# Optimization experiments

Hardware: AMD Instinct MI355X
Metric: run time of the kernel (lower is better)

## Reference

```python
import jax, jax.numpy as jnp
import numpy as np

DIM = 768
DEPTH = 12
HEADS = 12
DIM_HEAD = DIM // HEADS
DIM_MLP = 3072
PATCH = 16
SPECTRA = 4096
NUM_PATCHES = SPECTRA // PATCH
NUM_CLASSES = 1000
SCALE = DIM_HEAD ** -0.5
EPS = 1e-5


def sincos_pos_embed(embed_dim, n_pos):
    omega = np.arange(embed_dim // 2, dtype=np.float64) / (embed_dim / 2.0)
    omega = 1.0 / 10000 ** omega
    pos = np.arange(n_pos, dtype=np.float64)
    out = np.einsum('m,d->md', pos, omega)
    emb = np.concatenate([np.sin(out), np.cos(out)], axis=1)
    emb = np.concatenate([np.zeros([1, embed_dim]), emb], axis=0)  # cls slot
    return jnp.asarray(emb, jnp.float32)  # [N+1, D]


def setup_inputs() -> dict:
    key = jax.random.key(0)
    ks = jax.random.split(key, 12)
    s = 0.02
    d = {
        'x': jax.random.normal(ks[0], (32, 1, SPECTRA), jnp.float32),
        'conv_w': jax.random.normal(ks[1], (PATCH, DIM), jnp.float32) * s,
        'conv_b': jnp.zeros((DIM,), jnp.float32),
        'pos_embed': sincos_pos_embed(DIM, NUM_PATCHES),
        'cls_token': jax.random.normal(ks[2], (1, DIM), jnp.float32) * s,
        'ln1_w': jnp.ones((DEPTH, DIM), jnp.float32),
        'ln1_b': jnp.zeros((DEPTH, DIM), jnp.float32),
        'qkv_w': jax.random.normal(ks[3], (DEPTH, DIM, 3 * DIM), jnp.float32) * s,
        'out_w': jax.random.normal(ks[4], (DEPTH, DIM, DIM), jnp.float32) * s,
        'out_b': jnp.zeros((DEPTH, DIM), jnp.float32),
        'ln2_w': jnp.ones((DEPTH, DIM), jnp.float32),
        'ln2_b': jnp.zeros((DEPTH, DIM), jnp.float32),
        'mlp_w1': jax.random.normal(ks[5], (DEPTH, DIM, DIM_MLP), jnp.float32) * s,
        'mlp_b1': jnp.zeros((DEPTH, DIM_MLP), jnp.float32),
        'mlp_w2': jax.random.normal(ks[6], (DEPTH, DIM_MLP, DIM), jnp.float32) * s,
        'mlp_b2': jnp.zeros((DEPTH, DIM), jnp.float32),
        'cls_ln_w': jnp.ones((DIM,), jnp.float32),
        'cls_ln_b': jnp.zeros((DIM,), jnp.float32),
        'head_w': jax.random.normal(ks[7], (DIM, NUM_CLASSES), jnp.float32) * s,
        'head_b': jnp.zeros((NUM_CLASSES,), jnp.float32),
    }
    return d


def _ln(z, w, b):
    mu = z.mean(-1, keepdims=True)
    var = ((z - mu) ** 2).mean(-1, keepdims=True)
    return (z - mu) / jnp.sqrt(var + EPS) * w + b


def _forward(x, conv_w, conv_b, pos_embed, cls_token,
             ln1_w, ln1_b, qkv_w, out_w, out_b, ln2_w, ln2_b,
             mlp_w1, mlp_b1, mlp_w2, mlp_b2,
             cls_ln_w, cls_ln_b, head_w, head_b):
    B = x.shape[0]
    # Conv1d(1, D, k=P, stride=P) == non-overlapping patch linear proj
    patches = x.reshape(B, NUM_PATCHES, PATCH)
    h = patches @ conv_w + conv_b                         # [B, N, D]
    h = h + pos_embed[1:]
    cls = cls_token + pos_embed[:1]                       # [1, D]
    h = jnp.concatenate([jnp.broadcast_to(cls[None], (B, 1, DIM)), h], axis=1)  # [B, N+1, D]

    def block(h, p):
        l1w, l1b, qw, ow, ob, l2w, l2b, w1, b1, w2, b2 = p
        skip = h
        z = _ln(h, l1w, l1b)
        qkv = z @ qw                                      # [B, n, 3D]
        q, k, v = jnp.split(qkv, 3, axis=-1)
        def heads(t):
            return t.reshape(B, -1, HEADS, DIM_HEAD).transpose(0, 2, 1, 3)
        q, k, v = heads(q), heads(k), heads(v)            # [B, H, n, dh]
        dots = jnp.einsum('bhid,bhjd->bhij', q, k) * SCALE
        attn = jax.nn.softmax(dots, axis=-1)
        o = jnp.einsum('bhij,bhjd->bhid', attn, v)
        o = o.transpose(0, 2, 1, 3).reshape(B, -1, DIM)
        h = o @ ow + ob + skip
        skip = h
        z = _ln(h, l2w, l2b)
        z = jax.nn.gelu(z @ w1 + b1, approximate=False) @ w2 + b2
        return z + skip, None

    params = (ln1_w, ln1_b, qkv_w, out_w, out_b, ln2_w, ln2_b,
              mlp_w1, mlp_b1, mlp_w2, mlp_b2)
    h, _ = jax.lax.scan(block, h, params)
    cls_out = _ln(h[:, 0], cls_ln_w, cls_ln_b)
    return cls_out @ head_w + head_b                      # [B, num_classes]


def reference(x, conv_w, conv_b, pos_embed, cls_token,
              ln1_w, ln1_b, qkv_w, out_w, out_b, ln2_w, ln2_b,
              mlp_w1, mlp_b1, mlp_w2, mlp_b2,
              cls_ln_w, cls_ln_b, head_w, head_b):
    return _forward(x, conv_w, conv_b, pos_embed, cls_token,
                    ln1_w, ln1_b, qkv_w, out_w, out_b, ln2_w, ln2_b,
                    mlp_w1, mlp_b1, mlp_w2, mlp_b2,
                    cls_ln_w, cls_ln_b, head_w, head_b)
```

## Files before the change

kernel.cpp:

```cpp
#include <hip/hip_runtime.h>
#include <math.h>

#define DIM 768
#define DEPTH 12
#define HEADS 12
#define DIM_HEAD 64
#define DIM_MLP 3072
#define PATCH 16
#define NUM_PATCHES 256
#define SEQ 257
#define NUM_CLASSES 1000
#define BATCH 32
#define SCALE 0.125f
#define EPS 1e-5f
#define ROWS 8224
#define PAD_ROWS 8320
#define PAD_A 8448

typedef short bf16x8 __attribute__((ext_vector_type(8)));
typedef float f32x4 __attribute__((ext_vector_type(4)));

__device__ inline unsigned short f2bf(float f) {
    union { float f; unsigned int u; } c; c.f = f;
    unsigned int u = c.u;
    return (unsigned short)((u + 0x7fffu + ((u >> 16) & 1u)) >> 16);
}

#define MFMA16(d, a, b) d = __builtin_amdgcn_mfma_f32_16x16x32_bf16(a, b, d, 0, 0, 0)
#define SBAR() asm volatile("s_barrier" ::: "memory")
#define LGKM0() asm volatile("s_waitcnt lgkmcnt(0)" ::: "memory")

__global__ void patch_embed_kernel(const float* __restrict__ x,
                                   const float* __restrict__ conv_w,
                                   const float* __restrict__ conv_b,
                                   const float* __restrict__ pos,
                                   const float* __restrict__ cls_tok,
                                   float* __restrict__ h) {
    int row = blockIdx.x;
    int b = row / SEQ;
    int r = row % SEQ;
    int t = threadIdx.x;
    float* out = h + (long)row * DIM;
    if (r == 0) {
        for (int d = t; d < DIM; d += 256)
            out[d] = cls_tok[d] + pos[d];
        return;
    }
    int p = r - 1;
    const float* xp = x + (long)b * 4096 + p * PATCH;
    float xv[PATCH];
#pragma unroll
    for (int k = 0; k < PATCH; ++k) xv[k] = xp[k];
    for (int d = t; d < DIM; d += 256) {
        float acc = conv_b[d];
#pragma unroll
        for (int k = 0; k < PATCH; ++k)
            acc += xv[k] * conv_w[k * DIM + d];
        out[d] = acc + pos[(long)r * DIM + d];
    }
}

template <int OBF>
__global__ void layernorm_kernel(const float* __restrict__ in, long in_stride,
                                 const float* __restrict__ w,
                                 const float* __restrict__ bia,
                                 void* __restrict__ out) {
    __shared__ float red[8];
    long row = blockIdx.x;
    const float* src = in + row * in_stride;
    int t = threadIdx.x;
    float v0 = src[t], v1 = src[t + 256], v2 = src[t + 512];
    float s = v0 + v1 + v2;
    float q = v0 * v0 + v1 * v1 + v2 * v2;
#pragma unroll
    for (int off = 32; off; off >>= 1) {
        s += __shfl_down(s, off);
        q += __shfl_down(q, off);
    }
    if ((t & 63) == 0) { red[t >> 6] = s; red[4 + (t >> 6)] = q; }
    __syncthreads();
    if (t == 0) {
        float ss = red[0] + red[1] + red[2] + red[3];
        float qq = red[4] + red[5] + red[6] + red[7];
        float mu = ss * (1.0f / DIM);
        float var = qq * (1.0f / DIM) - mu * mu;
        red[0] = mu;
        red[1] = rsqrtf(var + EPS);
    }
    __syncthreads();
    float mu = red[0], rstd = red[1];
    float o0 = (v0 - mu) * rstd * w[t] + bia[t];
    float o1 = (v1 - mu) * rstd * w[t + 256] + bia[t + 256];
    float o2 = (v2 - mu) * rstd * w[t + 512] + bia[t + 512];
    if (OBF) {
        unsigned short* dst = (unsigned short*)out + row * DIM;
        dst[t] = f2bf(o0); dst[t + 256] = f2bf(o1); dst[t + 512] = f2bf(o2);
    } else {
        float* dst = (float*)out + row * DIM;
        dst[t] = o0; dst[t + 256] = o1; dst[t + 512] = o2;
    }
}

__global__ void transpose_all_kernel(const float* __restrict__ qw,
                                     const float* __restrict__ ow,
                                     const float* __restrict__ w1,
                                     const float* __restrict__ w2,
                                     unsigned short* __restrict__ qwT,
                                     unsigned short* __restrict__ owT,
                                     unsigned short* __restrict__ w1T,
                                     unsigned short* __restrict__ w2T) {
    __shared__ float tile[32][33];
    int t = blockIdx.x;
    const float* src; unsigned short* dst; int K, N, kt, nt;
    if (t < 1728)      {            src = qw; dst = qwT; K = 768;  N = 2304; kt = t % 24; nt = t / 24; }
    else if (t < 2304) { t -= 1728; src = ow; dst = owT; K = 768;  N = 768;  kt = t % 24; nt = t / 24; }
    else if (t < 4608) { t -= 2304; src = w1; dst = w1T; K = 768;  N = 3072; kt = t % 24; nt = t / 24; }
    else               { t -= 4608; src = w2; dst = w2T; K = 3072; N = 768;  kt = t % 96; nt = t / 96; }
    int k0 = kt * 32, n0 = nt * 32;
    int c = threadIdx.x & 31, r0 = threadIdx.x >> 5;
#pragma unroll
    for (int rr = r0; rr < 32; rr += 8)
        tile[rr][c] = src[(long)(k0 + rr) * N + n0 + c];
    __syncthreads();
#pragma unroll
    for (int rr = r0; rr < 32; rr += 8)
        dst[(long)(n0 + rr) * K + k0 + c] = f2bf(tile[c][rr]);
}

__global__ __launch_bounds__(256) void attn_kernel(const unsigned short* __restrict__ qkv,
                                                   unsigned short* __restrict__ o) {
    __shared__ unsigned short sh[60416];
    const int tid = threadIdx.x;
    const int lane = tid & 63;
    const int w = tid >> 6;

    const int nwg = gridDim.x;
    const int orig = blockIdx.x;
    const int q = nwg >> 3, r = nwg & 7;
    const int xcd = orig & 7, idx = orig >> 3;
    const int wg = (xcd < r ? xcd * (q + 1) : r * (q + 1) + (xcd - r) * q) + idx;
    const int bh = wg / 5, qt = wg % 5;
    const int b = bh / HEADS, hh = bh % HEADS;
    const unsigned short* qbase = qkv + (long)b * SEQ * 2304 + hh * 64;
    const unsigned short* kbase = qbase + 768;
    const unsigned short* vbase = qbase + 1536;

#pragma unroll
    for (int u = 0; u < 2; ++u) {
        int c = tid + u * 256;
        int j = c >> 3, cb = c & 7;
        int gj = qt * 64 + j; if (gj > 256) gj = 256;
        const unsigned short* g = qbase + (long)gj * 2304 + ((cb ^ (j & 7)) << 3);
        __builtin_amdgcn_global_load_lds(
            (const __attribute__((address_space(1))) void*)g,
            (__attribute__((address_space(3))) void*)&sh[j * 64 + cb * 8], 16, 0, 0);
    }
#pragma unroll
    for (int u = 0; u < 9; ++u) {
        int c = tid + u * 256;
        int j = c >> 3, cb = c & 7;
        int gj = j > 256 ? 256 : j;
        const unsigned short* g = kbase + (long)gj * 2304 + ((cb ^ (j & 7)) << 3);
        __builtin_amdgcn_global_load_lds(
            (const __attribute__((address_space(1))) void*)g,
            (__attribute__((address_space(3))) void*)&sh[4096 + j * 64 + cb * 8], 16, 0, 0);
    }
#pragma unroll
    for (int u = 0; u < 9; ++u) {
        int c = tid + u * 256;
        int j = c >> 3, dc = c & 7;
        short vv[8] = {0, 0, 0, 0, 0, 0, 0, 0};
        if (j < SEQ) *(bf16x8*)vv = *(const bf16x8*)(vbase + (long)j * 2304 + dc * 8);
#pragma unroll
        for (int e = 0; e < 8; ++e)
            sh[22528 + (dc * 8 + e) * 296 + j] = (unsigned short)vv[e];
    }
    __syncthreads();

    f32x4 s[18] = {};
#pragma unroll
    for (int ks = 0; ks < 2; ++ks) {
        int arow = w * 16 + (lane & 15);
        int cb = ks * 4 + (lane >> 4);
        bf16x8 aq = *(const bf16x8*)&sh[arow * 64 + ((cb ^ (arow & 7)) << 3)];
#pragma unroll
        for (int nf = 0; nf < 18; ++nf) {
            int brow = nf * 16 + (lane & 15);
            bf16x8 bk = *(const bf16x8*)&sh[4096 + brow * 64 + ((cb ^ (brow & 7)) << 3)];
            MFMA16(s[nf], aq, bk);
        }
    }

    float inv[4];
#pragma unroll
    for (int j = 0; j < 4; ++j) {
        float m_ = -3.0e38f;
#pragma unroll
        for (int nf = 0; nf < 18; ++nf) {
            int col = nf * 16 + (lane & 15);
            float x = (col < SEQ) ? s[nf][j] * SCALE : -3.0e38f;
            s[nf][j] = x;
            m_ = fmaxf(m_, x);
        }
#pragma unroll
        for (int off = 1; off < 16; off <<= 1) m_ = fmaxf(m_, __shfl_xor(m_, off));
        float sm = 0.f;
#pragma unroll
        for (int nf = 0; nf < 18; ++nf) {
            float e = __expf(s[nf][j] - m_);
            s[nf][j] = e;
            sm += e;
        }
#pragma unroll
        for (int off = 1; off < 16; off <<= 1) sm += __shfl_xor(sm, off);
        inv[j] = 1.0f / sm;
    }
#pragma unroll
    for (int nf = 0; nf < 18; ++nf) {
        int col = nf * 16 + (lane & 15);
#pragma unroll
        for (int j = 0; j < 4; ++j) {
            int row = w * 16 + (lane >> 4) * 4 + j;
            sh[41472 + row * 296 + col] = f2bf(s[nf][j] * inv[j]);
        }
    }
    __syncthreads();

    f32x4 oa[4] = {};
#pragma unroll
    for (int ks = 0; ks < 9; ++ks) {
        int prow = w * 16 + (lane & 15);
        bf16x8 ap = *(const bf16x8*)&sh[41472 + prow * 296 + ks * 32 + (lane >> 4) * 8];
#pragma unroll
        for (int n = 0; n < 4; ++n) {
            int drow = n * 16 + (lane & 15);
            bf16x8 bv = *(const bf16x8*)&sh[22528 + drow * 296 + ks * 32 + (lane >> 4) * 8];
            MFMA16(oa[n], ap, bv);
        }
    }
#pragma unroll
    for (int n = 0; n < 4; ++n) {
        int col = hh * 64 + n * 16 + (lane & 15);
#pragma unroll
        for (int j = 0; j < 4; ++j) {
            int gr = qt * 64 + w * 16 + (lane >> 4) * 4 + j;
            if (gr < SEQ)
                o[((long)(b * SEQ + gr)) * DIM + col] = f2bf(oa[n][j]);
        }
    }
}

template <int NK, int ACT, int OBF>
__global__ __launch_bounds__(256, 2) void gemmd_kernel(
    const unsigned short* __restrict__ A,
    const unsigned short* __restrict__ Bt,
    const float* __restrict__ bias,
    const float* __restrict__ resid,
    void* __restrict__ C,
    int M, int GY, int lda, int ldb, int ldc) {
    __shared__ unsigned short sh[32768];
    const int tid = threadIdx.x;
    const int lane = tid & 63;
    const int w = tid >> 6;
    const int wr = w >> 1, wc = w & 1;

    const int nwg = gridDim.x;
    const int orig = blockIdx.x;
    const int q = nwg >> 3, r = nwg & 7;
    const int xcd = orig & 7, idx = orig >> 3;
    const int wg = (xcd < r ? xcd * (q + 1) : r * (q + 1) + (xcd - r) * q) + idx;
    const int bm = (wg / GY) * 128;
    const int bn = (wg % GY) * 128;

    const unsigned short* Ag = A + (long)bm * lda;
    const unsigned short* Bg = Bt + (long)bn * ldb;

    auto stage = [&](int kt) {
        unsigned short* La = &sh[(kt & 1) * 16384];
        unsigned short* Lb = La + 8192;
#pragma unroll
        for (int u = 0; u < 4; ++u) {
            int c = tid + u * 256;
            int lr = c >> 3, cb = c & 7;
            int sw = (cb ^ (lr & 7)) << 3;
            const unsigned short* ga = Ag + (long)lr * lda + kt * 64 + sw;
            __builtin_amdgcn_global_load_lds(
                (const __attribute__((address_space(1))) void*)ga,
                (__attribute__((address_space(3))) void*)&La[lr * 64 + (cb << 3)], 16, 0, 0);
            const unsigned short* gb = Bg + (long)lr * ldb + kt * 64 + sw;
            __builtin_amdgcn_global_load_lds(
                (const __attribute__((address_space(1))) void*)gb,
                (__attribute__((address_space(3))) void*)&Lb[lr * 64 + (cb << 3)], 16, 0, 0);
        }
    };
    auto ldA = [&](int p, int m, int ks) {
        int row = wr * 64 + m * 16 + (lane & 15);
        int cb = ks * 4 + (lane >> 4);
        return *(const bf16x8*)&sh[p * 16384 + row * 64 + ((cb ^ (row & 7)) << 3)];
    };
    auto ldB = [&](int p, int n, int ks) {
        int row = wc * 64 + n * 16 + (lane & 15);
        int cb = ks * 4 + (lane >> 4);
        return *(const bf16x8*)&sh[p * 16384 + 8192 + row * 64 + ((cb ^ (row & 7)) << 3)];
    };

    f32x4 acc[4][4] = {};

    stage(0); stage(1);
    asm volatile("s_waitcnt vmcnt(8)" ::: "memory");
    SBAR();

    for (int kt = 0; kt < NK; ++kt) {
        const int p = kt & 1;
        bf16x8 a[4][2], b[4][2];
#pragma unroll
        for (int m = 0; m < 4; ++m) { a[m][0] = ldA(p, m, 0); a[m][1] = ldA(p, m, 1); }
#pragma unroll
        for (int n = 0; n < 4; ++n) { b[n][0] = ldB(p, n, 0); b[n][1] = ldB(p, n, 1); }
        SBAR();
        if (kt + 2 < NK) stage(kt + 2);
        LGKM0();
        __builtin_amdgcn_s_setprio(1);
#pragma unroll
        for (int m = 0; m < 4; ++m)
#pragma unroll
            for (int n = 0; n < 4; ++n) {
                MFMA16(acc[m][n], a[m][0], b[n][0]);
                MFMA16(acc[m][n], a[m][1], b[n][1]);
            }
        __builtin_amdgcn_s_setprio(0);
        if (kt + 2 < NK) {
            asm volatile("s_waitcnt vmcnt(8)" ::: "memory");
        } else if (kt + 1 < NK) {
            asm volatile("s_waitcnt vmcnt(0)" ::: "memory");
        }
        SBAR();
    }

#pragma unroll
    for (int mi = 0; mi < 4; ++mi) {
        int gr0 = bm + wr * 64 + mi * 16 + (lane >> 4) * 4;
#pragma unroll
        for (int ni = 0; ni < 4; ++ni) {
            int gc = bn + wc * 64 + ni * 16 + (lane & 15);
            float bv = bias ? bias[gc] : 0.f;
#pragma unroll
            for (int j = 0; j < 4; ++j) {
                int gr = gr0 + j;
                if (gr >= M) continue;
                float v = acc[mi][ni][j] + bv;
                if (ACT) v = 0.5f * v * (1.0f + erff(v * 0.70710678118654752f));
                long ci = (long)gr * ldc + gc;
                if (OBF) {
                    ((unsigned short*)C)[ci] = f2bf(v);
                } else {
                    if (resid) v += resid[ci];
                    ((float*)C)[ci] = v;
                }
            }
        }
    }
}

__global__ void gemm_f32_kernel(const float* __restrict__ A,
                                const float* __restrict__ W,
                                const float* __restrict__ bias,
                                float* __restrict__ C,
                                int M, int N, int K) {
    __shared__ float As[16][65];
    __shared__ float Bs[16][65];
    int bm = blockIdx.x * 64, bn = blockIdx.y * 64;
    int t = threadIdx.x;
    int tx = t & 15, ty = t >> 4;
    float acc[4][4] = {};
    for (int k0 = 0; k0 < K; k0 += 16) {
        {
            int ar = bm + (t >> 2);
            int ac = k0 + (t & 3) * 4;
            float4 av = make_float4(0.f, 0.f, 0.f, 0.f);
            if (ar < M) av = *(const float4*)(A + (long)ar * K + ac);
            int kk = (t & 3) * 4, rr = t >> 2;
            As[kk + 0][rr] = av.x; As[kk + 1][rr] = av.y;
            As[kk + 2][rr] = av.z; As[kk + 3][rr] = av.w;
        }
        {
            int wr2 = k0 + (t >> 4);
            int wc2 = bn + (t & 15) * 4;
            float4 wv;
            wv.x = (wc2 + 0 < N) ? W[(long)wr2 * N + wc2 + 0] : 0.f;
            wv.y = (wc2 + 1 < N) ? W[(long)wr2 * N + wc2 + 1] : 0.f;
            wv.z = (wc2 + 2 < N) ? W[(long)wr2 * N + wc2 + 2] : 0.f;
            wv.w = (wc2 + 3 < N) ? W[(long)wr2 * N + wc2 + 3] : 0.f;
            int kr = t >> 4, nc = (t & 15) * 4;
            Bs[kr][nc + 0] = wv.x; Bs[kr][nc + 1] = wv.y;
            Bs[kr][nc + 2] = wv.z; Bs[kr][nc + 3] = wv.w;
        }
        __syncthreads();
#pragma unroll
        for (int kk = 0; kk < 16; ++kk) {
            float a0 = As[kk][ty * 4 + 0], a1 = As[kk][ty * 4 + 1];
            float a2 = As[kk][ty * 4 + 2], a3 = As[kk][ty * 4 + 3];
            float b0 = Bs[kk][tx], b1 = Bs[kk][tx + 16];
            float b2 = Bs[kk][tx + 32], b3 = Bs[kk][tx + 48];
            acc[0][0] += a0 * b0; acc[0][1] += a0 * b1; acc[0][2] += a0 * b2; acc[0][3] += a0 * b3;
            acc[1][0] += a1 * b0; acc[1][1] += a1 * b1; acc[1][2] += a1 * b2; acc[1][3] += a1 * b3;
            acc[2][0] += a2 * b0; acc[2][1] += a2 * b1; acc[2][2] += a2 * b2; acc[2][3] += a2 * b3;
            acc[3][0] += a3 * b0; acc[3][1] += a3 * b1; acc[3][2] += a3 * b2; acc[3][3] += a3 * b3;
        }
        __syncthreads();
    }
#pragma unroll
    for (int i = 0; i < 4; ++i) {
        int r = bm + ty * 4 + i;
        if (r >= M) continue;
#pragma unroll
        for (int j = 0; j < 4; ++j) {
            int c = bn + tx + 16 * j;
            if (c >= N) continue;
            C[(long)r * N + c] = acc[i][j] + (bias ? bias[c] : 0.f);
        }
    }
}

extern "C" void kernel_launch(void* const* d_in, const int* in_sizes, int n_in,
                              void* d_out, int out_size, void* d_ws, size_t ws_size,
                              hipStream_t stream) {
    const float* x        = (const float*)d_in[0];
    const float* conv_w   = (const float*)d_in[1];
    const float* conv_b   = (const float*)d_in[2];
    const float* pos      = (const float*)d_in[3];
    const float* cls_tok  = (const float*)d_in[4];
    const float* ln1_w    = (const float*)d_in[5];
    const float* ln1_b    = (const float*)d_in[6];
    const float* qkv_w    = (const float*)d_in[7];
    const float* out_w    = (const float*)d_in[8];
    const float* out_b    = (const float*)d_in[9];
    const float* ln2_w    = (const float*)d_in[10];
    const float* ln2_b    = (const float*)d_in[11];
    const float* mlp_w1   = (const float*)d_in[12];
    const float* mlp_b1   = (const float*)d_in[13];
    const float* mlp_w2   = (const float*)d_in[14];
    const float* mlp_b2   = (const float*)d_in[15];
    const float* cls_ln_w = (const float*)d_in[16];
    const float* cls_ln_b = (const float*)d_in[17];
    const float* head_w   = (const float*)d_in[18];
    const float* head_b   = (const float*)d_in[19];
    float* out = (float*)d_out;

    char* cur = (char*)d_ws;
    auto alloc = [&](size_t bytes) {
        void* p = cur; cur += (bytes + 255) & ~(size_t)255; return p;
    };
    float*          h      = (float*)alloc((size_t)PAD_ROWS * DIM * 4);
    unsigned short* z_bf   = (unsigned short*)alloc((size_t)PAD_A * DIM * 2);
    unsigned short* qkv_bf = (unsigned short*)alloc((size_t)ROWS * 3 * DIM * 2);
    unsigned short* o_bf   = (unsigned short*)alloc((size_t)PAD_ROWS * DIM * 2);
    unsigned short* m1     = (unsigned short*)alloc((size_t)PAD_ROWS * DIM_MLP * 2);
    unsigned short* qkvwT  = (unsigned short*)alloc((size_t)2304 * 768 * 2);
    unsigned short* owT    = (unsigned short*)alloc((size_t)768 * 768 * 2);
    unsigned short* w1T    = (unsigned short*)alloc((size_t)3072 * 768 * 2);
    unsigned short* w2T    = (unsigned short*)alloc((size_t)768 * 3072 * 2);
    float*          clsz   = (float*)alloc((size_t)BATCH * DIM * 4);

    patch_embed_kernel<<<ROWS, 256, 0, stream>>>(x, conv_w, conv_b, pos, cls_tok, h);

    for (int l = 0; l < DEPTH; ++l) {
        transpose_all_kernel<<<6912, 256, 0, stream>>>(
            qkv_w + (long)l * DIM * 3 * DIM, out_w + (long)l * DIM * DIM,
            mlp_w1 + (long)l * DIM * DIM_MLP, mlp_w2 + (long)l * DIM_MLP * DIM,
            qkvwT, owT, w1T, w2T);

        layernorm_kernel<1><<<ROWS, 256, 0, stream>>>(
            h, DIM, ln1_w + (long)l * DIM, ln1_b + (long)l * DIM, z_bf);

        gemmd_kernel<12, 0, 1><<<65 * 18, 256, 0, stream>>>(
            z_bf, qkvwT, nullptr, nullptr, qkv_bf, ROWS, 18, DIM, DIM, 3 * DIM);

        attn_kernel<<<384 * 5, 256, 0, stream>>>(qkv_bf, o_bf);

        gemmd_kernel<12, 0, 0><<<65 * 6, 256, 0, stream>>>(
            o_bf, owT, out_b + (long)l * DIM, h, h, ROWS, 6, DIM, DIM, DIM);

        layernorm_kernel<1><<<ROWS, 256, 0, stream>>>(
            h, DIM, ln2_w + (long)l * DIM, ln2_b + (long)l * DIM, z_bf);

        gemmd_kernel<12, 1, 1><<<65 * 24, 256, 0, stream>>>(
            z_bf, w1T, mlp_b1 + (long)l * DIM_MLP, nullptr, m1, ROWS, 24, DIM, DIM, DIM_MLP);

        gemmd_kernel<48, 0, 0><<<65 * 6, 256, 0, stream>>>(
            m1, w2T, mlp_b2 + (long)l * DIM, h, h, ROWS, 6, DIM_MLP, DIM_MLP, DIM);
    }

    layernorm_kernel<0><<<BATCH, 256, 0, stream>>>(
        h, (long)SEQ * DIM, cls_ln_w, cls_ln_b, clsz);
    gemm_f32_kernel<<<dim3(1, 16), 256, 0, stream>>>(
        clsz, head_w, head_b, out, BATCH, NUM_CLASSES, DIM);
}
```

Baseline: 4.404 ms.

## Deepen GEMM pipeline to 4-stage K=32 buffers and batch weight transposes

The GEMM main loop changes from a 2-buffer, K=64-per-stage scheme to a 4-buffer ring with K=32 per stage, prefetching three stages ahead so more global loads are in flight while MFMAs run. When workspace allows, all 12 layers' weights are transposed to bf16 in one large launch instead of one launch per layer, cutting launch count and letting the transposes run as a single wide kernel. The shallower K per stage halves the MFMA work between barriers, which may add synchronization overhead. The vmcnt bookkeeping for the tail iterations is also adjusted.

```diff
diff --git a/kernel.cpp b/kernel.cpp
--- a/kernel.cpp
+++ b/kernel.cpp
@@ -17,6 +17,12 @@
 #define PAD_ROWS 8320
 #define PAD_A 8448
 
+#define WL_QKV 0
+#define WL_OW  (2304 * 768)
+#define WL_W1  (WL_OW + 768 * 768)
+#define WL_W2  (WL_W1 + 3072 * 768)
+#define WL_TOT (WL_W2 + 768 * 3072)
+
 typedef short bf16x8 __attribute__((ext_vector_type(8)));
 typedef float f32x4 __attribute__((ext_vector_type(4)));
 
@@ -101,21 +107,21 @@
     }
 }
 
+template <int LAYERS>
 __global__ void transpose_all_kernel(const float* __restrict__ qw,
                                      const float* __restrict__ ow,
                                      const float* __restrict__ w1,
                                      const float* __restrict__ w2,
-                                     unsigned short* __restrict__ qwT,
-                                     unsigned short* __restrict__ owT,
-                                     unsigned short* __restrict__ w1T,
-                                     unsigned short* __restrict__ w2T) {
+                                     unsigned short* __restrict__ wOut) {
     __shared__ float tile[32][33];
     int t = blockIdx.x;
+    int l = t / 6912; t -= l * 6912;
     const float* src; unsigned short* dst; int K, N, kt, nt;
-    if (t < 1728)      {            src = qw; dst = qwT; K = 768;  N = 2304; kt = t % 24; nt = t / 24; }
-    else if (t < 2304) { t -= 1728; src = ow; dst = owT; K = 768;  N = 768;  kt = t % 24; nt = t / 24; }
-    else if (t < 4608) { t -= 2304; src = w1; dst = w1T; K = 768;  N = 3072; kt = t % 24; nt = t / 24; }
-    else               { t -= 4608; src = w2; dst = w2T; K = 3072; N = 768;  kt = t % 96; nt = t / 96; }
+    unsigned short* wL = wOut + (long)l * WL_TOT;
+    if (t < 1728)      {            src = qw + (long)l * 768 * 2304; dst = wL + WL_QKV; K = 768;  N = 2304; kt = t % 24; nt = t / 24; }
+    else if (t < 2304) { t -= 1728; src = ow + (long)l * 768 * 768;  dst = wL + WL_OW;  K = 768;  N = 768;  kt = t % 24; nt = t / 24; }
+    else if (t < 4608) { t -= 2304; src = w1 + (long)l * 768 * 3072; dst = wL + WL_W1;  K = 768;  N = 3072; kt = t % 24; nt = t / 24; }
+    else               { t -= 4608; src = w2 + (long)l * 3072 * 768; dst = wL + WL_W2;  K = 3072; N = 768;  kt = t % 96; nt = t / 96; }
     int k0 = kt * 32, n0 = nt * 32;
     int c = threadIdx.x & 31, r0 = threadIdx.x >> 5;
 #pragma unroll
@@ -276,61 +282,59 @@
     const unsigned short* Bg = Bt + (long)bn * ldb;
 
     auto stage = [&](int kt) {
-        unsigned short* La = &sh[(kt & 1) * 16384];
-        unsigned short* Lb = La + 8192;
-#pragma unroll
-        for (int u = 0; u < 4; ++u) {
+        unsigned short* La = &sh[(kt & 3) * 8192];
+#pragma unroll
+        for (int u = 0; u < 2; ++u) {
             int c = tid + u * 256;
-            int lr = c >> 3, cb = c & 7;
-            int sw = (cb ^ (lr & 7)) << 3;
-            const unsigned short* ga = Ag + (long)lr * lda + kt * 64 + sw;
+            int lr = c >> 2, cb = c & 3;
+            int sw = (cb ^ (lr & 3)) << 3;
+            const unsigned short* ga = Ag + (long)lr * lda + kt * 32 + sw;
             __builtin_amdgcn_global_load_lds(
                 (const __attribute__((address_space(1))) void*)ga,
-                (__attribute__((address_space(3))) void*)&La[lr * 64 + (cb << 3)], 16, 0, 0);
-            const unsigned short* gb = Bg + (long)lr * ldb + kt * 64 + sw;
+                (__attribute__((address_space(3))) void*)&La[lr * 32 + (cb << 3)], 16, 0, 0);
+            const unsigned short* gb = Bg + (long)lr * ldb + kt * 32 + sw;
             __builtin_amdgcn_global_load_lds(
                 (const __attribute__((address_space(1))) void*)gb,
-                (__attribute__((address_space(3))) void*)&Lb[lr * 64 + (cb << 3)], 16, 0, 0);
+                (__attribute__((address_space(3))) void*)&La[4096 + lr * 32 + (cb << 3)], 16, 0, 0);
         }
     };
-    auto ldA = [&](int p, int m, int ks) {
+    auto ldA = [&](int kt, int m) {
         int row = wr * 64 + m * 16 + (lane & 15);
-        int cb = ks * 4 + (lane >> 4);
-        return *(const bf16x8*)&sh[p * 16384 + row * 64 + ((cb ^ (row & 7)) << 3)];
+        int cb = lane >> 4;
+        return *(const bf16x8*)&sh[(kt & 3) * 8192 + row * 32 + ((cb ^ (row & 3)) << 3)];
     };
-    auto ldB = [&](int p, int n, int ks) {
+    auto ldB = [&](int kt, int n) {
         int row = wc * 64 + n * 16 + (lane & 15);
-        int cb = ks * 4 + (lane >> 4);
-        return *(const bf16x8*)&sh[p * 16384 + 8192 + row * 64 + ((cb ^ (row & 7)) << 3)];
+        int cb = lane >> 4;
+        return *(const bf16x8*)&sh[(kt & 3) * 8192 + 4096 + row * 32 + ((cb ^ (row & 3)) << 3)];
     };
 
     f32x4 acc[4][4] = {};
 
-    stage(0); stage(1);
+    stage(0); stage(1); stage(2);
     asm volatile("s_waitcnt vmcnt(8)" ::: "memory");
     SBAR();
 
     for (int kt = 0; kt < NK; ++kt) {
-        const int p = kt & 1;
-        bf16x8 a[4][2], b[4][2];
-#pragma unroll
-        for (int m = 0; m < 4; ++m) { a[m][0] = ldA(p, m, 0); a[m][1] = ldA(p, m, 1); }
-#pragma unroll
-        for (int n = 0; n < 4; ++n) { b[n][0] = ldB(p, n, 0); b[n][1] = ldB(p, n, 1); }
+        bf16x8 a[4], b[4];
+#pragma unroll
+        for (int m = 0; m < 4; ++m) a[m] = ldA(kt, m);
+#pragma unroll
+        for (int n = 0; n < 4; ++n) b[n] = ldB(kt, n);
         SBAR();
-        if (kt + 2 < NK) stage(kt + 2);
+        if (kt + 3 < NK) stage(kt + 3);
         LGKM0();
         __builtin_amdgcn_s_setprio(1);
 #pragma unroll
         for (int m = 0; m < 4; ++m)
 #pragma unroll
-            for (int n = 0; n < 4; ++n) {
-                MFMA16(acc[m][n], a[m][0], b[n][0]);
-                MFMA16(acc[m][n], a[m][1], b[n][1]);
-            }
+            for (int n = 0; n < 4; ++n)
+                MFMA16(acc[m][n], a[m], b[n]);
         __builtin_amdgcn_s_setprio(0);
-        if (kt + 2 < NK) {
+        if (kt + 3 < NK) {
             asm volatile("s_waitcnt vmcnt(8)" ::: "memory");
+        } else if (kt + 2 < NK) {
+            asm volatile("s_waitcnt vmcnt(4)" ::: "memory");
         } else if (kt + 1 < NK) {
             asm volatile("s_waitcnt vmcnt(0)" ::: "memory");
         }
@@ -456,38 +460,46 @@
     unsigned short* qkv_bf = (unsigned short*)alloc((size_t)ROWS * 3 * DIM * 2);
     unsigned short* o_bf   = (unsigned short*)alloc((size_t)PAD_ROWS * DIM * 2);
     unsigned short* m1     = (unsigned short*)alloc((size_t)PAD_ROWS * DIM_MLP * 2);
-    unsigned short* qkvwT  = (unsigned short*)alloc((size_t)2304 * 768 * 2);
-    unsigned short* owT    = (unsigned short*)alloc((size_t)768 * 768 * 2);
-    unsigned short* w1T    = (unsigned short*)alloc((size_t)3072 * 768 * 2);
-    unsigned short* w2T    = (unsigned short*)alloc((size_t)768 * 3072 * 2);
     float*          clsz   = (float*)alloc((size_t)BATCH * DIM * 4);
+    size_t used = (size_t)(cur - (char*)d_ws);
+    bool all_layers = (ws_size - used) >= (size_t)12 * WL_TOT * 2 + 256;
+    unsigned short* wAll = (unsigned short*)alloc((all_layers ? (size_t)12 : (size_t)1) * WL_TOT * 2);
 
     patch_embed_kernel<<<ROWS, 256, 0, stream>>>(x, conv_w, conv_b, pos, cls_tok, h);
 
+    if (all_layers)
+        transpose_all_kernel<12><<<12 * 6912, 256, 0, stream>>>(
+            qkv_w, out_w, mlp_w1, mlp_w2, wAll);
+
     for (int l = 0; l < DEPTH; ++l) {
-        transpose_all_kernel<<<6912, 256, 0, stream>>>(
-            qkv_w + (long)l * DIM * 3 * DIM, out_w + (long)l * DIM * DIM,
-            mlp_w1 + (long)l * DIM * DIM_MLP, mlp_w2 + (long)l * DIM_MLP * DIM,
-            qkvwT, owT, w1T, w2T);
+        unsigned short* wL = wAll + (all_layers ? (long)l * WL_TOT : 0);
+        if (!all_layers)
+            transpose_all_kernel<1><<<6912, 256, 0, stream>>>(
+                qkv_w + (long)l * DIM * 3 * DIM, out_w + (long)l * DIM * DIM,
+                mlp_w1 + (long)l * DIM * DIM_MLP, mlp_w2 + (long)l * DIM_MLP * DIM, wL);
+        unsigned short* qkvwT = wL + WL_QKV;
+        unsigned short* owT   = wL + WL_OW;
+        unsigned short* w1T   = wL + WL_W1;
+        unsigned short* w2T   = wL + WL_W2;
 
         layernorm_kernel<1><<<ROWS, 256, 0, stream>>>(
             h, DIM, ln1_w + (long)l * DIM, ln1_b + (long)l * DIM, z_bf);
 
-        gemmd_kernel<12, 0, 1><<<65 * 18, 256, 0, stream>>>(
+        gemmd_kernel<24, 0, 1><<<65 * 18, 256, 0, stream>>>(
             z_bf, qkvwT, nullptr, nullptr, qkv_bf, ROWS, 18, DIM, DIM, 3 * DIM);
 
         attn_kernel<<<384 * 5, 256, 0, stream>>>(qkv_bf, o_bf);
 
-        gemmd_kernel<12, 0, 0><<<65 * 6, 256, 0, stream>>>(
+        gemmd_kernel<24, 0, 0><<<65 * 6, 256, 0, stream>>>(
             o_bf, owT, out_b + (long)l * DIM, h, h, ROWS, 6, DIM, DIM, DIM);
 
         layernorm_kernel<1><<<ROWS, 256, 0, stream>>>(
             h, DIM, ln2_w + (long)l * DIM, ln2_b + (long)l * DIM, z_bf);
 
-        gemmd_kernel<12, 1, 1><<<65 * 24, 256, 0, stream>>>(
+        gemmd_kernel<24, 1, 1><<<65 * 24, 256, 0, stream>>>(
             z_bf, w1T, mlp_b1 + (long)l * DIM_MLP, nullptr, m1, ROWS, 24, DIM, DIM, DIM_MLP);
 
-        gemmd_kernel<48, 0, 0><<<65 * 6, 256, 0, stream>>>(
+        gemmd_kernel<96, 0, 0><<<65 * 6, 256, 0, stream>>>(
             m1, w2T, mlp_b2 + (long)l * DIM, h, h, ROWS, 6, DIM_MLP, DIM_MLP, DIM);
     }
 
```

New measurement: 4.755 ms. 1.08x slower.

## Batch weight transposes across layers and widen attention workgroups to 128 query rows

Applied to the files above, without the earlier changes.

Weight transposition and bf16 conversion for all 12 layers now runs in one launch up front when the workspace is large enough, replacing twelve per-layer launches. The attention kernel now uses 512-thread workgroups covering 128 query rows each, in 3 tiles per batch-head instead of 5 tiles of 64. This means K and V are loaded into LDS and V is transposed fewer times per head. Q is now read straight from global memory into registers instead of through LDS. The wider blocks need more LDS per workgroup, which may reduce occupancy.

```diff
diff --git a/kernel.cpp b/kernel.cpp
--- a/kernel.cpp
+++ b/kernel.cpp
@@ -17,6 +17,12 @@
 #define PAD_ROWS 8320
 #define PAD_A 8448
 
+#define WL_QKV 0
+#define WL_OW  (2304 * 768)
+#define WL_W1  (WL_OW + 768 * 768)
+#define WL_W2  (WL_W1 + 3072 * 768)
+#define WL_TOT (WL_W2 + 768 * 3072)
+
 typedef short bf16x8 __attribute__((ext_vector_type(8)));
 typedef float f32x4 __attribute__((ext_vector_type(4)));
 
@@ -101,21 +107,21 @@
     }
 }
 
+template <int LAYERS>
 __global__ void transpose_all_kernel(const float* __restrict__ qw,
                                      const float* __restrict__ ow,
                                      const float* __restrict__ w1,
                                      const float* __restrict__ w2,
-                                     unsigned short* __restrict__ qwT,
-                                     unsigned short* __restrict__ owT,
-                                     unsigned short* __restrict__ w1T,
-                                     unsigned short* __restrict__ w2T) {
+                                     unsigned short* __restrict__ wOut) {
     __shared__ float tile[32][33];
     int t = blockIdx.x;
+    int l = t / 6912; t -= l * 6912;
     const float* src; unsigned short* dst; int K, N, kt, nt;
-    if (t < 1728)      {            src = qw; dst = qwT; K = 768;  N = 2304; kt = t % 24; nt = t / 24; }
-    else if (t < 2304) { t -= 1728; src = ow; dst = owT; K = 768;  N = 768;  kt = t % 24; nt = t / 24; }
-    else if (t < 4608) { t -= 2304; src = w1; dst = w1T; K = 768;  N = 3072; kt = t % 24; nt = t / 24; }
-    else               { t -= 4608; src = w2; dst = w2T; K = 3072; N = 768;  kt = t % 96; nt = t / 96; }
+    unsigned short* wL = wOut + (long)l * WL_TOT;
+    if (t < 1728)      {            src = qw + (long)l * 768 * 2304; dst = wL + WL_QKV; K = 768;  N = 2304; kt = t % 24; nt = t / 24; }
+    else if (t < 2304) { t -= 1728; src = ow + (long)l * 768 * 768;  dst = wL + WL_OW;  K = 768;  N = 768;  kt = t % 24; nt = t / 24; }
+    else if (t < 4608) { t -= 2304; src = w1 + (long)l * 768 * 3072; dst = wL + WL_W1;  K = 768;  N = 3072; kt = t % 24; nt = t / 24; }
+    else               { t -= 4608; src = w2 + (long)l * 3072 * 768; dst = wL + WL_W2;  K = 3072; N = 768;  kt = t % 96; nt = t / 96; }
     int k0 = kt * 32, n0 = nt * 32;
     int c = threadIdx.x & 31, r0 = threadIdx.x >> 5;
 #pragma unroll
@@ -127,9 +133,9 @@
         dst[(long)(n0 + rr) * K + k0 + c] = f2bf(tile[c][rr]);
 }
 
-__global__ __launch_bounds__(256) void attn_kernel(const unsigned short* __restrict__ qkv,
-                                                   unsigned short* __restrict__ o) {
-    __shared__ unsigned short sh[60416];
+__global__ __launch_bounds__(512) void attn2_kernel(const unsigned short* __restrict__ qkv,
+                                                    unsigned short* __restrict__ o) {
+    __shared__ unsigned short sh[75264];
     const int tid = threadIdx.x;
     const int lane = tid & 63;
     const int w = tid >> 6;
@@ -139,54 +145,49 @@
     const int q = nwg >> 3, r = nwg & 7;
     const int xcd = orig & 7, idx = orig >> 3;
     const int wg = (xcd < r ? xcd * (q + 1) : r * (q + 1) + (xcd - r) * q) + idx;
-    const int bh = wg / 5, qt = wg % 5;
+    const int bh = wg / 3, qc = wg % 3;
     const int b = bh / HEADS, hh = bh % HEADS;
     const unsigned short* qbase = qkv + (long)b * SEQ * 2304 + hh * 64;
     const unsigned short* kbase = qbase + 768;
     const unsigned short* vbase = qbase + 1536;
 
 #pragma unroll
-    for (int u = 0; u < 2; ++u) {
-        int c = tid + u * 256;
-        int j = c >> 3, cb = c & 7;
-        int gj = qt * 64 + j; if (gj > 256) gj = 256;
-        const unsigned short* g = qbase + (long)gj * 2304 + ((cb ^ (j & 7)) << 3);
-        __builtin_amdgcn_global_load_lds(
-            (const __attribute__((address_space(1))) void*)g,
-            (__attribute__((address_space(3))) void*)&sh[j * 64 + cb * 8], 16, 0, 0);
-    }
-#pragma unroll
-    for (int u = 0; u < 9; ++u) {
-        int c = tid + u * 256;
-        int j = c >> 3, cb = c & 7;
-        int gj = j > 256 ? 256 : j;
-        const unsigned short* g = kbase + (long)gj * 2304 + ((cb ^ (j & 7)) << 3);
-        __builtin_amdgcn_global_load_lds(
-            (const __attribute__((address_space(1))) void*)g,
-            (__attribute__((address_space(3))) void*)&sh[4096 + j * 64 + cb * 8], 16, 0, 0);
-    }
-#pragma unroll
-    for (int u = 0; u < 9; ++u) {
-        int c = tid + u * 256;
-        int j = c >> 3, dc = c & 7;
-        short vv[8] = {0, 0, 0, 0, 0, 0, 0, 0};
-        if (j < SEQ) *(bf16x8*)vv = *(const bf16x8*)(vbase + (long)j * 2304 + dc * 8);
-#pragma unroll
-        for (int e = 0; e < 8; ++e)
-            sh[22528 + (dc * 8 + e) * 296 + j] = (unsigned short)vv[e];
+    for (int u = 0; u < 5; ++u) {
+        int c = tid + u * 512;
+        if (c < 2304) {
+            int j = c >> 3, cb = c & 7;
+            int gj = j > 256 ? 256 : j;
+            const unsigned short* g = kbase + (long)gj * 2304 + ((cb ^ (j & 7)) << 3);
+            __builtin_amdgcn_global_load_lds(
+                (const __attribute__((address_space(1))) void*)g,
+                (__attribute__((address_space(3))) void*)&sh[j * 64 + cb * 8], 16, 0, 0);
+        }
+    }
+#pragma unroll
+    for (int u = 0; u < 5; ++u) {
+        int c = tid + u * 512;
+        if (c < 2304) {
+            int j = c >> 3, dc = c & 7;
+            short vv[8] = {0, 0, 0, 0, 0, 0, 0, 0};
+            if (j < SEQ) *(bf16x8*)vv = *(const bf16x8*)(vbase + (long)j * 2304 + dc * 8);
+#pragma unroll
+            for (int e = 0; e < 8; ++e)
+                sh[18432 + (dc * 8 + e) * 296 + j] = (unsigned short)vv[e];
+        }
     }
     __syncthreads();
 
+    const int arow = qc * 128 + w * 16 + (lane & 15);
+    const int garow = arow > 256 ? 256 : arow;
     f32x4 s[18] = {};
 #pragma unroll
     for (int ks = 0; ks < 2; ++ks) {
-        int arow = w * 16 + (lane & 15);
+        bf16x8 aq = *(const bf16x8*)(qbase + (long)garow * 2304 + ks * 32 + (lane >> 4) * 8);
         int cb = ks * 4 + (lane >> 4);
-        bf16x8 aq = *(const bf16x8*)&sh[arow * 64 + ((cb ^ (arow & 7)) << 3)];
 #pragma unroll
         for (int nf = 0; nf < 18; ++nf) {
             int brow = nf * 16 + (lane & 15);
-            bf16x8 bk = *(const bf16x8*)&sh[4096 + brow * 64 + ((cb ^ (brow & 7)) << 3)];
+            bf16x8 bk = *(const bf16x8*)&sh[brow * 64 + ((cb ^ (brow & 7)) << 3)];
             MFMA16(s[nf], aq, bk);
         }
     }
@@ -198,9 +199,9 @@
 #pragma unroll
         for (int nf = 0; nf < 18; ++nf) {
             int col = nf * 16 + (lane & 15);
-            float x = (col < SEQ) ? s[nf][j] * SCALE : -3.0e38f;
-            s[nf][j] = x;
-            m_ = fmaxf(m_, x);
+            float xv = (col < SEQ) ? s[nf][j] * SCALE : -3.0e38f;
+            s[nf][j] = xv;
+            m_ = fmaxf(m_, xv);
         }
 #pragma unroll
         for (int off = 1; off < 16; off <<= 1) m_ = fmaxf(m_, __shfl_xor(m_, off));
@@ -221,20 +222,20 @@
 #pragma unroll
         for (int j = 0; j < 4; ++j) {
             int row = w * 16 + (lane >> 4) * 4 + j;
-            sh[41472 + row * 296 + col] = f2bf(s[nf][j] * inv[j]);
+            sh[37376 + row * 296 + col] = f2bf(s[nf][j] * inv[j]);
         }
     }
     __syncthreads();
 
     f32x4 oa[4] = {};
+    const int prow = w * 16 + (lane & 15);
 #pragma unroll
     for (int ks = 0; ks < 9; ++ks) {
-        int prow = w * 16 + (lane & 15);
-        bf16x8 ap = *(const bf16x8*)&sh[41472 + prow * 296 + ks * 32 + (lane >> 4) * 8];
+        bf16x8 ap = *(const bf16x8*)&sh[37376 + prow * 296 + ks * 32 + (lane >> 4) * 8];
 #pragma unroll
         for (int n = 0; n < 4; ++n) {
             int drow = n * 16 + (lane & 15);
-            bf16x8 bv = *(const bf16x8*)&sh[22528 + drow * 296 + ks * 32 + (lane >> 4) * 8];
+            bf16x8 bv = *(const bf16x8*)&sh[18432 + drow * 296 + ks * 32 + (lane >> 4) * 8];
             MFMA16(oa[n], ap, bv);
         }
     }
@@ -243,7 +244,7 @@
         int col = hh * 64 + n * 16 + (lane & 15);
 #pragma unroll
         for (int j = 0; j < 4; ++j) {
-            int gr = qt * 64 + w * 16 + (lane >> 4) * 4 + j;
+            int gr = qc * 128 + w * 16 + (lane >> 4) * 4 + j;
             if (gr < SEQ)
                 o[((long)(b * SEQ + gr)) * DIM + col] = f2bf(oa[n][j]);
         }
@@ -456,19 +457,27 @@
     unsigned short* qkv_bf = (unsigned short*)alloc((size_t)ROWS * 3 * DIM * 2);
     unsigned short* o_bf   = (unsigned short*)alloc((size_t)PAD_ROWS * DIM * 2);
     unsigned short* m1     = (unsigned short*)alloc((size_t)PAD_ROWS * DIM_MLP * 2);
-    unsigned short* qkvwT  = (unsigned short*)alloc((size_t)2304 * 768 * 2);
-    unsigned short* owT    = (unsigned short*)alloc((size_t)768 * 768 * 2);
-    unsigned short* w1T    = (unsigned short*)alloc((size_t)3072 * 768 * 2);
-    unsigned short* w2T    = (unsigned short*)alloc((size_t)768 * 3072 * 2);
     float*          clsz   = (float*)alloc((size_t)BATCH * DIM * 4);
+    size_t used = (size_t)(cur - (char*)d_ws);
+    bool all_layers = (ws_size - used) >= (size_t)12 * WL_TOT * 2 + 256;
+    unsigned short* wAll = (unsigned short*)alloc((all_layers ? (size_t)12 : (size_t)1) * WL_TOT * 2);
 
     patch_embed_kernel<<<ROWS, 256, 0, stream>>>(x, conv_w, conv_b, pos, cls_tok, h);
 
+    if (all_layers)
+        transpose_all_kernel<12><<<12 * 6912, 256, 0, stream>>>(
+            qkv_w, out_w, mlp_w1, mlp_w2, wAll);
+
     for (int l = 0; l < DEPTH; ++l) {
-        transpose_all_kernel<<<6912, 256, 0, stream>>>(
-            qkv_w + (long)l * DIM * 3 * DIM, out_w + (long)l * DIM * DIM,
-            mlp_w1 + (long)l * DIM * DIM_MLP, mlp_w2 + (long)l * DIM_MLP * DIM,
-            qkvwT, owT, w1T, w2T);
+        unsigned short* wL = wAll + (all_layers ? (long)l * WL_TOT : 0);
+        if (!all_layers)
+            transpose_all_kernel<1><<<6912, 256, 0, stream>>>(
+                qkv_w + (long)l * DIM * 3 * DIM, out_w + (long)l * DIM * DIM,
+                mlp_w1 + (long)l * DIM * DIM_MLP, mlp_w2 + (long)l * DIM_MLP * DIM, wL);
+        unsigned short* qkvwT = wL + WL_QKV;
+        unsigned short* owT   = wL + WL_OW;
+        unsigned short* w1T   = wL + WL_W1;
+        unsigned short* w2T   = wL + WL_W2;
 
         layernorm_kernel<1><<<ROWS, 256, 0, stream>>>(
             h, DIM, ln1_w + (long)l * DIM, ln1_b + (long)l * DIM, z_bf);
@@ -476,7 +485,7 @@
         gemmd_kernel<12, 0, 1><<<65 * 18, 256, 0, stream>>>(
             z_bf, qkvwT, nullptr, nullptr, qkv_bf, ROWS, 18, DIM, DIM, 3 * DIM);
 
-        attn_kernel<<<384 * 5, 256, 0, stream>>>(qkv_bf, o_bf);
+        attn2_kernel<<<384 * 3, 512, 0, stream>>>(qkv_bf, o_bf);
 
         gemmd_kernel<12, 0, 0><<<65 * 6, 256, 0, stream>>>(
             o_bf, owT, out_b + (long)l * DIM, h, h, ROWS, 6, DIM, DIM, DIM);
```

Measured after the change: 4.232 ms. -3.9%, faster.
